# Kernel tuning notes

Measured on AMD Instinct MI355X. Metric: run time of the kernel, lower is better.

The kernel has to match this reference:

```python
import jax, jax.numpy as jnp
import numpy as np

N = 50000
E = 800000
IN_DIM = 256
OUT_DIM = 32
HEADS = 4
HC = OUT_DIM * HEADS  # 128
NEG_SLOPE = 0.2


def _gat_conv(x, src, dst, edge_attr, W, att_src, att_dst, W_e, att_e, b):
    """PyG GATConv (concat=True, edge_dim given, eval mode). src/dst already
    include self loops; edge_attr is [E', 1] with mean-filled self-loop attrs."""
    n = x.shape[0]
    h = (x @ W).reshape(n, HEADS, OUT_DIM)                 # [N,H,C]
    a_s = (h * att_src).sum(-1)                             # [N,H]
    a_d = (h * att_dst).sum(-1)                             # [N,H]
    e = (edge_attr @ W_e).reshape(-1, HEADS, OUT_DIM)       # [E',H,C]
    a_e = (e * att_e).sum(-1)                               # [E',H]
    alpha = jax.nn.leaky_relu(a_s[src] + a_d[dst] + a_e, NEG_SLOPE)
    # softmax over incoming edges per destination node
    m = jax.ops.segment_max(alpha, dst, num_segments=n)
    ex = jnp.exp(alpha - m[dst])
    denom = jax.ops.segment_sum(ex, dst, num_segments=n)
    w = ex / denom[dst]                                     # [E',H]
    out = jax.ops.segment_sum(w[:, :, None] * h[src], dst, num_segments=n)
    return out.reshape(n, HC) + b


def setup_inputs() -> dict:
    key = jax.random.key(0)
    ks = jax.random.split(key, 16)
    x = jax.random.normal(ks[0], (N, IN_DIM), dtype=jnp.float32)
    src = jax.random.randint(ks[1], (E,), 0, N)
    # guarantee no self loops (PyG removes then re-adds them)
    off = jax.random.randint(ks[2], (E,), 1, N)
    dst = (src + off) % N
    edge_index = jnp.stack([src, dst]).astype(jnp.int64)
    edge_weight = jax.random.uniform(ks[3], (E,), dtype=jnp.float32)
    s = 0.1
    params = {
        "W1": jax.random.normal(ks[4], (IN_DIM, HC), jnp.float32) * s,
        "att_src1": jax.random.normal(ks[5], (HEADS, OUT_DIM), jnp.float32) * s,
        "att_dst1": jax.random.normal(ks[6], (HEADS, OUT_DIM), jnp.float32) * s,
        "W_e1": jax.random.normal(ks[7], (1, HC), jnp.float32) * s,
        "att_e1": jax.random.normal(ks[8], (HEADS, OUT_DIM), jnp.float32) * s,
        "b1": jnp.zeros((HC,), jnp.float32),
        "W2": jax.random.normal(ks[9], (HC, HC), jnp.float32) * s,
        "att_src2": jax.random.normal(ks[10], (HEADS, OUT_DIM), jnp.float32) * s,
        "att_dst2": jax.random.normal(ks[11], (HEADS, OUT_DIM), jnp.float32) * s,
        "W_e2": jax.random.normal(ks[12], (1, HC), jnp.float32) * s,
        "att_e2": jax.random.normal(ks[13], (HEADS, OUT_DIM), jnp.float32) * s,
        "b2": jnp.zeros((HC,), jnp.float32),
    }
    return {"x": x, "edge_index": edge_index, "edge_weight": edge_weight, **params}


def reference(x, edge_index, edge_weight,
              W1, att_src1, att_dst1, W_e1, att_e1, b1,
              W2, att_src2, att_dst2, W_e2, att_e2, b2):
    ew = edge_weight[:, None]                               # [E,1]
    # add self loops; self-loop edge_attr = mean of edge_attr (fill_value='mean')
    loop = jnp.arange(N, dtype=edge_index.dtype)
    src = jnp.concatenate([edge_index[0], loop])
    dst = jnp.concatenate([edge_index[1], loop])
    ea = jnp.concatenate([ew, jnp.broadcast_to(ew.mean(0, keepdims=True), (N, 1))])
    h1 = _gat_conv(x, src, dst, ea, W1, att_src1, att_dst1, W_e1, att_e1, b1)
    h2 = _gat_conv(h1, src, dst, ea, W2, att_src2, att_dst2, W_e2, att_e2, b2)
    return h2
```

## Files before the change

### kernel.cpp

```cpp
#include <hip/hip_runtime.h>
#include <hip/hip_fp16.h>

#define N_NODES 50000
#define N_EDGES 800000
#define E_TOT   850000
#define HC 128
#define NEG_SLOPE 0.2f
#define TILE 128
#define KP 40
#define CH 4096
#define NCH ((E_TOT + CH - 1) / CH)
#define NP  ((N_NODES + 255) >> 8)

typedef unsigned short u16;
typedef __attribute__((ext_vector_type(8))) short short8;
typedef __attribute__((ext_vector_type(4))) float f32x4;

__device__ __forceinline__ int edge_get(const void* eidx, int f64, long long i) {
  return f64 ? (int)((const long long*)eidx)[i] : ((const int*)eidx)[i];
}
__device__ __forceinline__ float selh(float4 q, int head) {
  float a = (head & 1) ? q.y : q.x;
  float b = (head & 1) ? q.w : q.z;
  return (head & 2) ? b : a;
}
__device__ __forceinline__ float4 alpha4(float4 as, float4 ad, float w, float4 c) {
  float4 r;
  r.x = as.x + ad.x + w * c.x; r.x = r.x > 0.f ? r.x : NEG_SLOPE * r.x;
  r.y = as.y + ad.y + w * c.y; r.y = r.y > 0.f ? r.y : NEG_SLOPE * r.y;
  r.z = as.z + ad.z + w * c.z; r.z = r.z > 0.f ? r.z : NEG_SLOPE * r.z;
  r.w = as.w + ad.w + w * c.w; r.w = r.w > 0.f ? r.w : NEG_SLOPE * r.w;
  return r;
}
__device__ __forceinline__ void wave_max4(float4& m) {
  #pragma unroll
  for (int o = 1; o < 64; o <<= 1) {
    m.x = fmaxf(m.x, __shfl_xor(m.x, o, 64));
    m.y = fmaxf(m.y, __shfl_xor(m.y, o, 64));
    m.z = fmaxf(m.z, __shfl_xor(m.z, o, 64));
    m.w = fmaxf(m.w, __shfl_xor(m.w, o, 64));
  }
}
__device__ __forceinline__ void wave_sum4(float4& s) {
  #pragma unroll
  for (int o = 1; o < 64; o <<= 1) {
    s.x += __shfl_xor(s.x, o, 64);
    s.y += __shfl_xor(s.y, o, 64);
    s.z += __shfl_xor(s.z, o, 64);
    s.w += __shfl_xor(s.w, o, 64);
  }
}
__device__ __forceinline__ void splitbf(float v, u16& h, u16& l) {
  unsigned b = __float_as_uint(v);
  h = (u16)(b >> 16);
  float lo = v - __uint_as_float(b & 0xFFFF0000u);
  l = (u16)(__float_as_uint(lo) >> 16);
}
__device__ __forceinline__ int block_scan_excl(int val, int* lds) {
  int lane = threadIdx.x & 63, wv = threadIdx.x >> 6;
  int inc = val;
  #pragma unroll
  for (int off = 1; off < 64; off <<= 1) {
    int t = __shfl_up(inc, off, 64);
    if (lane >= off) inc += t;
  }
  if (lane == 63) lds[wv] = inc;
  __syncthreads();
  if (threadIdx.x == 0) {
    int s = 0;
    #pragma unroll
    for (int i = 0; i < 4; ++i) { int t = lds[i]; lds[i] = s; s += t; }
  }
  __syncthreads();
  return lds[wv] + inc - val;
}

__global__ void detect_kernel(const void* eidx, int* flag) {
  const long long* p = (const long long*)eidx;
  long long v = p[threadIdx.x];
  int bad = (v < 0 || v >= N_NODES);
  unsigned long long anybad = __ballot(bad);
  if (threadIdx.x == 0) *flag = (anybad == 0ull);
}

__global__ __launch_bounds__(256) void chunkhist_kernel(const void* eidx,
    const int* __restrict__ flag, const float* __restrict__ ew,
    int* __restrict__ cnt, float* __restrict__ scal) {
  __shared__ int hist[NP];
  __shared__ float sh[4];
  int c = blockIdx.x, tid = threadIdx.x;
  for (int i = tid; i < NP; i += 256) hist[i] = 0;
  __syncthreads();
  int f = *flag;
  int i0 = c * CH, i1 = min(i0 + CH, E_TOT);
  float s = 0.f;
  for (int i = i0 + tid; i < i1; i += 256) {
    int d = (i < N_EDGES) ? edge_get(eidx, f, (long long)N_EDGES + i) : (i - N_EDGES);
    atomicAdd(&hist[d >> 8], 1);
    if (i < N_EDGES) s += ew[i];
  }
  #pragma unroll
  for (int m = 32; m >= 1; m >>= 1) s += __shfl_xor(s, m, 64);
  int lane = tid & 63, wv = tid >> 6;
  if (lane == 0) sh[wv] = s;
  __syncthreads();
  for (int i = tid; i < NP; i += 256) cnt[c * NP + i] = hist[i];
  if (tid == 0) atomicAdd(&scal[0], sh[0] + sh[1] + sh[2] + sh[3]);
}

__global__ __launch_bounds__(256) void colscan_kernel(const int* __restrict__ cnt,
    int* __restrict__ base_rel, int* __restrict__ ptot) {
  __shared__ int lds[4];
  int p = blockIdx.x, c = threadIdx.x;
  int v = (c < NCH) ? cnt[c * NP + p] : 0;
  int e = block_scan_excl(v, lds);
  if (c < NCH) base_rel[c * NP + p] = e;
  if (c == 255) ptot[p] = e;
}

__global__ __launch_bounds__(256) void pscan_prep_kernel(const int* __restrict__ ptot,
    int* __restrict__ pofs, const float* __restrict__ We1, const float* __restrict__ ae1,
    const float* __restrict__ We2, const float* __restrict__ ae2,
    float* __restrict__ scal, float inv_e) {
  __shared__ int lds[4];
  int t = threadIdx.x;
  int v = (t < NP) ? ptot[t] : 0;
  int e = block_scan_excl(v, lds);
  if (t <= NP) pofs[t] = e;
  float p = (t < 128) ? We1[t] * ae1[t] : We2[t - 128] * ae2[t - 128];
  #pragma unroll
  for (int m = 16; m >= 1; m >>= 1) p += __shfl_xor(p, m, 32);
  if ((t & 31) == 0) {
    int hd = (t & 127) >> 5;
    if (t < 128) scal[4 + hd] = p; else scal[8 + hd] = p;
  }
  if (t == 0) scal[1] = scal[0] * inv_e;
}

__global__ __launch_bounds__(256) void partition_kernel(const void* eidx,
    const int* __restrict__ flag, const float* __restrict__ ew,
    const float* __restrict__ scal, const int* __restrict__ base_rel,
    const int* __restrict__ pofs, int2* __restrict__ swp1) {
  __shared__ int cur[NP];
  int c = blockIdx.x, tid = threadIdx.x;
  for (int i = tid; i < NP; i += 256) cur[i] = base_rel[c * NP + i] + pofs[i];
  __syncthreads();
  int f = *flag;
  float wmean = scal[1];
  int i0 = c * CH, i1 = min(i0 + CH, E_TOT);
  for (int i = i0 + tid; i < i1; i += 256) {
    int s, d; float w;
    if (i < N_EDGES) {
      s = edge_get(eidx, f, i);
      d = edge_get(eidx, f, (long long)N_EDGES + i);
      w = ew[i];
    } else {
      s = d = i - N_EDGES;
      w = wmean;
    }
    int pos = atomicAdd(&cur[d >> 8], 1);
    swp1[pos] = make_int2((int)(((unsigned)d << 16) | (unsigned)s), __float_as_int(w));
  }
}

__global__ __launch_bounds__(256) void localsort_kernel(const int2* __restrict__ swp1,
    const int* __restrict__ pofs, int* __restrict__ offs, int2* __restrict__ swp2) {
  __shared__ int lhist[256];
  __shared__ int lds[4];
  int p = blockIdx.x, tid = threadIdx.x;
  int r0 = pofs[p], r1 = pofs[p + 1];
  lhist[tid] = 0;
  __syncthreads();
  for (int i = r0 + tid; i < r1; i += 256) {
    unsigned key = (unsigned)swp1[i].x;
    atomicAdd(&lhist[(key >> 16) & 255u], 1);
  }
  __syncthreads();
  int v = lhist[tid];
  int e = block_scan_excl(v, lds);
  int node = (p << 8) + tid;
  if (node < N_NODES) offs[node] = r0 + e;
  if (p == 0 && tid == 0) offs[N_NODES] = E_TOT;
  lhist[tid] = e;
  __syncthreads();
  for (int i = r0 + tid; i < r1; i += 256) {
    int2 rec = swp1[i];
    unsigned key = (unsigned)rec.x;
    int pos = r0 + atomicAdd(&lhist[(key >> 16) & 255u], 1);
    swp2[pos] = make_int2((int)(key & 0xFFFFu), rec.y);
  }
}

__global__ __launch_bounds__(256) void wprep_kernel(const float* __restrict__ W1,
    const float* __restrict__ W2, u16* __restrict__ w1h, u16* __restrict__ w1l,
    u16* __restrict__ w2h, u16* __restrict__ w2l) {
  int i = blockIdx.x * 256 + threadIdx.x;
  if (i < 128 * 256) {
    int ch = i >> 8, k = i & 255;
    u16 h, l; splitbf(W1[k * 128 + ch], h, l);
    w1h[i] = h; w1l[i] = l;
  } else if (i < 128 * 256 + 128 * 128) {
    int j = i - 128 * 256;
    int ch = j >> 7, k = j & 127;
    u16 h, l; splitbf(W2[k * 128 + ch], h, l);
    w2h[j] = h; w2l[j] = l;
  }
}

__global__ __launch_bounds__(256) void mfma_gemm_kernel(const float* __restrict__ A,
    const u16* __restrict__ wth, const u16* __restrict__ wtl,
    __half* __restrict__ h16, int M, int K) {
  __shared__ u16 Xh[128][KP], Xl[128][KP];
  __shared__ u16 Gh[128][KP], Gl[128][KP];
  int tid  = threadIdx.x;
  int lane = tid & 63, wid = tid >> 6;
  int q = lane >> 4, r = lane & 15;
  int wm = wid >> 1, wn = wid & 1;
  int node0 = blockIdx.x * 128;
  int srow  = tid >> 1;
  int skoff = (tid & 1) << 4;

  f32x4 acc[4][4];
  #pragma unroll
  for (int i = 0; i < 4; ++i)
    #pragma unroll
    for (int j = 0; j < 4; ++j) acc[i][j] = (f32x4)0.f;

  for (int k0 = 0; k0 < K; k0 += 32) {
    int gn = node0 + srow;
    float xv[16];
    if (gn < M) {
      const float* src = A + (size_t)gn * K + k0 + skoff;
      #pragma unroll
      for (int j = 0; j < 4; ++j) {
        float4 t = *(const float4*)(src + j * 4);
        xv[j * 4 + 0] = t.x; xv[j * 4 + 1] = t.y;
        xv[j * 4 + 2] = t.z; xv[j * 4 + 3] = t.w;
      }
    } else {
      #pragma unroll
      for (int j = 0; j < 16; ++j) xv[j] = 0.f;
    }
    const u16* wsrc = wth + (size_t)srow * K + k0 + skoff;
    const u16* lsrc = wtl + (size_t)srow * K + k0 + skoff;
    short8 wh0 = *(const short8*)wsrc;
    short8 wh1 = *(const short8*)(wsrc + 8);
    short8 wl0 = *(const short8*)lsrc;
    short8 wl1 = *(const short8*)(lsrc + 8);
    __syncthreads();
    short8 xh0, xh1, xl0, xl1;
    #pragma unroll
    for (int j = 0; j < 8; ++j) {
      u16 h, l;
      splitbf(xv[j], h, l);     xh0[j] = (short)h; xl0[j] = (short)l;
      splitbf(xv[j + 8], h, l); xh1[j] = (short)h; xl1[j] = (short)l;
    }
    *(short8*)&Xh[srow][skoff]     = xh0;
    *(short8*)&Xh[srow][skoff + 8] = xh1;
    *(short8*)&Xl[srow][skoff]     = xl0;
    *(short8*)&Xl[srow][skoff + 8] = xl1;
    *(short8*)&Gh[srow][skoff]     = wh0;
    *(short8*)&Gh[srow][skoff + 8] = wh1;
    *(short8*)&Gl[srow][skoff]     = wl0;
    *(short8*)&Gl[srow][skoff + 8] = wl1;
    __syncthreads();
    short8 ah[4], al[4], bh[4], bl[4];
    #pragma unroll
    for (int mi = 0; mi < 4; ++mi) {
      int row = wm * 64 + mi * 16 + r;
      ah[mi] = *(const short8*)&Gh[row][q * 8];
      al[mi] = *(const short8*)&Gl[row][q * 8];
    }
    #pragma unroll
    for (int ni = 0; ni < 4; ++ni) {
      int row = wn * 64 + ni * 16 + r;
      bh[ni] = *(const short8*)&Xh[row][q * 8];
      bl[ni] = *(const short8*)&Xl[row][q * 8];
    }
    #pragma unroll
    for (int mi = 0; mi < 4; ++mi)
      #pragma unroll
      for (int ni = 0; ni < 4; ++ni) {
        acc[mi][ni] = __builtin_amdgcn_mfma_f32_16x16x32_bf16(ah[mi], bh[ni], acc[mi][ni], 0, 0, 0);
        acc[mi][ni] = __builtin_amdgcn_mfma_f32_16x16x32_bf16(ah[mi], bl[ni], acc[mi][ni], 0, 0, 0);
        acc[mi][ni] = __builtin_amdgcn_mfma_f32_16x16x32_bf16(al[mi], bh[ni], acc[mi][ni], 0, 0, 0);
      }
  }
  #pragma unroll
  for (int ni = 0; ni < 4; ++ni) {
    int node = node0 + wn * 64 + ni * 16 + r;
    if (node < M) {
      #pragma unroll
      for (int mi = 0; mi < 4; ++mi) {
        int chb = wm * 64 + mi * 16 + q * 4;
        __half hh[4];
        hh[0] = __float2half(acc[mi][ni][0]);
        hh[1] = __float2half(acc[mi][ni][1]);
        hh[2] = __float2half(acc[mi][ni][2]);
        hh[3] = __float2half(acc[mi][ni][3]);
        *(float2*)(h16 + (size_t)node * HC + chb) = *(float2*)hh;
      }
    }
  }
}

__global__ __launch_bounds__(256) void attn_coef16_kernel(const __half* __restrict__ h,
    const float* __restrict__ att_s, const float* __restrict__ att_d,
    float* __restrict__ a_s, float* __restrict__ a_d, int n) {
  int lane = threadIdx.x & 63, wid = threadIdx.x >> 6;
  int node = blockIdx.x * 4 + wid;
  if (node >= n) return;
  __half2 hv = *(const __half2*)(h + (size_t)node * HC + 2 * lane);
  float v0 = __low2float(hv), v1 = __high2float(hv);
  float2 as2 = *(const float2*)(att_s + 2 * lane);
  float2 ad2 = *(const float2*)(att_d + 2 * lane);
  float ps = v0 * as2.x + v1 * as2.y;
  float pd = v0 * ad2.x + v1 * ad2.y;
  #pragma unroll
  for (int o = 1; o < 16; o <<= 1) {
    ps += __shfl_xor(ps, o, 64);
    pd += __shfl_xor(pd, o, 64);
  }
  if ((lane & 15) == 0) {
    a_s[(size_t)node * 4 + (lane >> 4)] = ps;
    a_d[(size_t)node * 4 + (lane >> 4)] = pd;
  }
}

__global__ __launch_bounds__(256) void aggregate_kernel(const __half* __restrict__ h,
    const int2* __restrict__ swp, const int* __restrict__ offs,
    const float* __restrict__ a_s, const float* __restrict__ a_d,
    const float* __restrict__ cptr, const float* __restrict__ bias,
    float* __restrict__ out, int n) {
  __shared__ float4 wals[4][TILE];
  __shared__ int    ssh[4][TILE];
  int lane = threadIdx.x & 63;
  int wv   = threadIdx.x >> 6;
  int v    = blockIdx.x * 4 + wv;
  if (v >= n) return;
  int r0  = offs[v];
  int deg = offs[v + 1] - r0;
  float4 c  = *(const float4*)cptr;
  float4 ad = *(const float4*)(a_d + (size_t)v * 4);
  int head  = lane >> 4;
  float2 acc = make_float2(0.f, 0.f);
  const __half* hb = h + 2 * lane;
  float4 mx = make_float4(-INFINITY, -INFINITY, -INFINITY, -INFINITY);
  float4 sm = make_float4(0.f, 0.f, 0.f, 0.f);

  if (deg <= TILE) {
    for (int i = lane; i < deg; i += 64) {
      int2 sw = swp[r0 + i];
      float w = __int_as_float(sw.y);
      float4 as = *(const float4*)(a_s + (size_t)sw.x * 4);
      float4 al = alpha4(as, ad, w, c);
      wals[wv][i] = al; ssh[wv][i] = sw.x;
      mx.x = fmaxf(mx.x, al.x); mx.y = fmaxf(mx.y, al.y);
      mx.z = fmaxf(mx.z, al.z); mx.w = fmaxf(mx.w, al.w);
    }
    wave_max4(mx);
    for (int i = lane; i < deg; i += 64) {
      float4 al = wals[wv][i];
      float4 e;
      e.x = expf(al.x - mx.x); e.y = expf(al.y - mx.y);
      e.z = expf(al.z - mx.z); e.w = expf(al.w - mx.w);
      wals[wv][i] = e;
      sm.x += e.x; sm.y += e.y; sm.z += e.z; sm.w += e.w;
    }
    wave_sum4(sm);
    int i = 0;
    for (; i + 8 <= deg; i += 8) {
      float wr[8]; int sr[8];
      #pragma unroll
      for (int j = 0; j < 8; ++j) {
        sr[j] = ssh[wv][i + j];
        wr[j] = ((const float*)&wals[wv][i + j])[head];
      }
      __half2 hv[8];
      #pragma unroll
      for (int j = 0; j < 8; ++j)
        hv[j] = *(const __half2*)(hb + (size_t)sr[j] * HC);
      #pragma unroll
      for (int j = 0; j < 8; ++j) {
        acc.x += wr[j] * __low2float(hv[j]);
        acc.y += wr[j] * __high2float(hv[j]);
      }
    }
    for (; i < deg; ++i) {
      int s0 = ssh[wv][i];
      float w0 = ((const float*)&wals[wv][i])[head];
      __half2 hvv = *(const __half2*)(hb + (size_t)s0 * HC);
      acc.x += w0 * __low2float(hvv);
      acc.y += w0 * __high2float(hvv);
    }
  } else {
    for (int i = lane; i < deg; i += 64) {
      int2 sw = swp[r0 + i];
      float4 as = *(const float4*)(a_s + (size_t)sw.x * 4);
      float4 al = alpha4(as, ad, __int_as_float(sw.y), c);
      mx.x = fmaxf(mx.x, al.x); mx.y = fmaxf(mx.y, al.y);
      mx.z = fmaxf(mx.z, al.z); mx.w = fmaxf(mx.w, al.w);
    }
    wave_max4(mx);
    for (int i = lane; i < deg; i += 64) {
      int2 sw = swp[r0 + i];
      float4 as = *(const float4*)(a_s + (size_t)sw.x * 4);
      float4 al = alpha4(as, ad, __int_as_float(sw.y), c);
      sm.x += expf(al.x - mx.x); sm.y += expf(al.y - mx.y);
      sm.z += expf(al.z - mx.z); sm.w += expf(al.w - mx.w);
    }
    wave_sum4(sm);
    float mxh = selh(mx, head);
    for (int i = 0; i < deg; ++i) {
      int2 sw = swp[r0 + i];
      float4 as = *(const float4*)(a_s + (size_t)sw.x * 4);
      float4 al = alpha4(as, ad, __int_as_float(sw.y), c);
      float e = expf(selh(al, head) - mxh);
      __half2 hvv = *(const __half2*)(hb + (size_t)sw.x * HC);
      acc.x += e * __low2float(hvv);
      acc.y += e * __high2float(hvv);
    }
  }
  float inv = 1.0f / selh(sm, head);
  float2 bb = *(const float2*)(bias + 2 * lane);
  float2 r;
  r.x = acc.x * inv + bb.x;
  r.y = acc.y * inv + bb.y;
  *(float2*)(out + (size_t)v * HC + 2 * lane) = r;
}

extern "C" void kernel_launch(void* const* d_in, const int* in_sizes, int n_in,
                              void* d_out, int out_size, void* d_ws, size_t ws_size,
                              hipStream_t stream) {
  const float* x   = (const float*)d_in[0];
  const void*  ei  = d_in[1];
  const float* ew  = (const float*)d_in[2];
  const float* W1  = (const float*)d_in[3];
  const float* as1 = (const float*)d_in[4];
  const float* ad1 = (const float*)d_in[5];
  const float* We1 = (const float*)d_in[6];
  const float* ae1 = (const float*)d_in[7];
  const float* b1  = (const float*)d_in[8];
  const float* W2  = (const float*)d_in[9];
  const float* as2 = (const float*)d_in[10];
  const float* ad2 = (const float*)d_in[11];
  const float* We2 = (const float*)d_in[12];
  const float* ae2 = (const float*)d_in[13];
  const float* b2  = (const float*)d_in[14];
  float* out = (float*)d_out;

  char* p = (char*)d_ws;
  auto alloc = [&](size_t b) { char* r = p; p += (b + 255) & ~(size_t)255; return r; };
  float*  scal     = (float*)alloc(256);
  __half* h16      = (__half*)alloc((size_t)N_NODES * HC * 2);
  float*  out1     = (float*)alloc((size_t)N_NODES * HC * 4);
  float*  a_s      = (float*)alloc((size_t)N_NODES * 4 * 4);
  float*  a_d      = (float*)alloc((size_t)N_NODES * 4 * 4);
  int*    offs     = (int*)alloc((size_t)(N_NODES + 1) * 4);
  int*    cnt      = (int*)alloc((size_t)NCH * NP * 4);
  int*    base_rel = (int*)alloc((size_t)NCH * NP * 4);
  int*    ptot     = (int*)alloc((size_t)NP * 4);
  int*    pofs     = (int*)alloc((size_t)(NP + 1) * 4);
  int2*   swp1     = (int2*)alloc((size_t)E_TOT * 8);
  int2*   swp2     = (int2*)alloc((size_t)E_TOT * 8);
  u16*    w1h      = (u16*)alloc((size_t)128 * 256 * 2);
  u16*    w1l      = (u16*)alloc((size_t)128 * 256 * 2);
  u16*    w2h      = (u16*)alloc((size_t)128 * 128 * 2);
  u16*    w2l      = (u16*)alloc((size_t)128 * 128 * 2);

  hipMemsetAsync(scal, 0, 256, stream);

  int* flag = (int*)scal + 16;

  detect_kernel<<<1, 64, 0, stream>>>(ei, flag);
  chunkhist_kernel<<<NCH, 256, 0, stream>>>(ei, flag, ew, cnt, scal);
  colscan_kernel<<<NP, 256, 0, stream>>>(cnt, base_rel, ptot);
  pscan_prep_kernel<<<1, 256, 0, stream>>>(ptot, pofs, We1, ae1, We2, ae2, scal,
                                           1.0f / N_EDGES);
  partition_kernel<<<NCH, 256, 0, stream>>>(ei, flag, ew, scal, base_rel, pofs, swp1);
  localsort_kernel<<<NP, 256, 0, stream>>>(swp1, pofs, offs, swp2);
  wprep_kernel<<<192, 256, 0, stream>>>(W1, W2, w1h, w1l, w2h, w2l);

  const int ggrid = (N_NODES + 127) / 128;
  const int agrid = (N_NODES + 3) / 4;
  mfma_gemm_kernel<<<ggrid, 256, 0, stream>>>(x, w1h, w1l, h16, N_NODES, 256);
  attn_coef16_kernel<<<agrid, 256, 0, stream>>>(h16, as1, ad1, a_s, a_d, N_NODES);
  aggregate_kernel<<<agrid, 256, 0, stream>>>(h16, swp2, offs, a_s, a_d, scal + 4, b1,
                                              out1, N_NODES);
  mfma_gemm_kernel<<<ggrid, 256, 0, stream>>>(out1, w2h, w2l, h16, N_NODES, 128);
  attn_coef16_kernel<<<agrid, 256, 0, stream>>>(h16, as2, ad2, a_s, a_d, N_NODES);
  aggregate_kernel<<<agrid, 256, 0, stream>>>(h16, swp2, offs, a_s, a_d, scal + 8, b2,
                                              out, N_NODES);
}
```

Before: 298.7 us.

## Fuse attention coefficients into GEMM epilogue, inline index detection, widen gather unroll

Computes the per-node a_s/a_d attention dot products directly from the MFMA accumulators in the GEMM epilogue, which removes the separate attn_coef kernel and its reread of h16. The index-dtype detection kernel is folded into chunkhist and partition, so each block redoes a 64-element check instead of paying for an extra launch. The aggregate gather loop now unrolls 16 loads per step with masked tails instead of 8 plus a scalar remainder, aiming for more memory parallelism. The trade-offs are a heavier GEMM epilogue with extra registers and shuffles, and some wasted loads on the padded tail of short neighbour lists.

```diff
diff --git a/kernel.cpp b/kernel.cpp
--- a/kernel.cpp
+++ b/kernel.cpp
@@ -74,24 +74,26 @@
   __syncthreads();
   return lds[wv] + inc - val;
 }
-
-__global__ void detect_kernel(const void* eidx, int* flag) {
-  const long long* p = (const long long*)eidx;
-  long long v = p[threadIdx.x];
-  int bad = (v < 0 || v >= N_NODES);
-  unsigned long long anybad = __ballot(bad);
-  if (threadIdx.x == 0) *flag = (anybad == 0ull);
+__device__ __forceinline__ int local_detect(const void* eidx, int* f_sh) {
+  int tid = threadIdx.x;
+  if (tid < 64) {
+    long long v = ((const long long*)eidx)[tid];
+    int bad = (v < 0 || v >= N_NODES);
+    unsigned long long anybad = __ballot(bad);
+    if (tid == 0) *f_sh = (anybad == 0ull);
+  }
+  __syncthreads();
+  return *f_sh;
 }
 
 __global__ __launch_bounds__(256) void chunkhist_kernel(const void* eidx,
-    const int* __restrict__ flag, const float* __restrict__ ew,
-    int* __restrict__ cnt, float* __restrict__ scal) {
+    const float* __restrict__ ew, int* __restrict__ cnt, float* __restrict__ scal) {
   __shared__ int hist[NP];
   __shared__ float sh[4];
+  __shared__ int f_sh;
   int c = blockIdx.x, tid = threadIdx.x;
   for (int i = tid; i < NP; i += 256) hist[i] = 0;
-  __syncthreads();
-  int f = *flag;
+  int f = local_detect(eidx, &f_sh);
   int i0 = c * CH, i1 = min(i0 + CH, E_TOT);
   float s = 0.f;
   for (int i = i0 + tid; i < i1; i += 256) {
@@ -138,14 +140,14 @@
 }
 
 __global__ __launch_bounds__(256) void partition_kernel(const void* eidx,
-    const int* __restrict__ flag, const float* __restrict__ ew,
-    const float* __restrict__ scal, const int* __restrict__ base_rel,
-    const int* __restrict__ pofs, int2* __restrict__ swp1) {
+    const float* __restrict__ ew, const float* __restrict__ scal,
+    const int* __restrict__ base_rel, const int* __restrict__ pofs,
+    int2* __restrict__ swp1) {
   __shared__ int cur[NP];
+  __shared__ int f_sh;
   int c = blockIdx.x, tid = threadIdx.x;
   for (int i = tid; i < NP; i += 256) cur[i] = base_rel[c * NP + i] + pofs[i];
-  __syncthreads();
-  int f = *flag;
+  int f = local_detect(eidx, &f_sh);
   float wmean = scal[1];
   int i0 = c * CH, i1 = min(i0 + CH, E_TOT);
   for (int i = i0 + tid; i < i1; i += 256) {
@@ -209,7 +211,9 @@
 
 __global__ __launch_bounds__(256) void mfma_gemm_kernel(const float* __restrict__ A,
     const u16* __restrict__ wth, const u16* __restrict__ wtl,
-    __half* __restrict__ h16, int M, int K) {
+    const float* __restrict__ att_s, const float* __restrict__ att_d,
+    __half* __restrict__ h16, float* __restrict__ a_s, float* __restrict__ a_d,
+    int M, int K) {
   __shared__ u16 Xh[128][KP], Xl[128][KP];
   __shared__ u16 Gh[128][KP], Gl[128][KP];
   int tid  = threadIdx.x;
@@ -286,6 +290,12 @@
         acc[mi][ni] = __builtin_amdgcn_mfma_f32_16x16x32_bf16(al[mi], bh[ni], acc[mi][ni], 0, 0, 0);
       }
   }
+  float4 sv[4], dv[4];
+  #pragma unroll
+  for (int mi = 0; mi < 4; ++mi) {
+    sv[mi] = *(const float4*)(att_s + wm * 64 + mi * 16 + q * 4);
+    dv[mi] = *(const float4*)(att_d + wm * 64 + mi * 16 + q * 4);
+  }
   #pragma unroll
   for (int ni = 0; ni < 4; ++ni) {
     int node = node0 + wn * 64 + ni * 16 + r;
@@ -301,29 +311,31 @@
         *(float2*)(h16 + (size_t)node * HC + chb) = *(float2*)hh;
       }
     }
-  }
-}
-
-__global__ __launch_bounds__(256) void attn_coef16_kernel(const __half* __restrict__ h,
-    const float* __restrict__ att_s, const float* __restrict__ att_d,
-    float* __restrict__ a_s, float* __restrict__ a_d, int n) {
-  int lane = threadIdx.x & 63, wid = threadIdx.x >> 6;
-  int node = blockIdx.x * 4 + wid;
-  if (node >= n) return;
-  __half2 hv = *(const __half2*)(h + (size_t)node * HC + 2 * lane);
-  float v0 = __low2float(hv), v1 = __high2float(hv);
-  float2 as2 = *(const float2*)(att_s + 2 * lane);
-  float2 ad2 = *(const float2*)(att_d + 2 * lane);
-  float ps = v0 * as2.x + v1 * as2.y;
-  float pd = v0 * ad2.x + v1 * ad2.y;
-  #pragma unroll
-  for (int o = 1; o < 16; o <<= 1) {
-    ps += __shfl_xor(ps, o, 64);
-    pd += __shfl_xor(pd, o, 64);
-  }
-  if ((lane & 15) == 0) {
-    a_s[(size_t)node * 4 + (lane >> 4)] = ps;
-    a_d[(size_t)node * 4 + (lane >> 4)] = pd;
+    float ps0 = 0.f, pd0 = 0.f, ps1 = 0.f, pd1 = 0.f;
+    #pragma unroll
+    for (int mi = 0; mi < 2; ++mi)
+      #pragma unroll
+      for (int t = 0; t < 4; ++t) {
+        float av = acc[mi][ni][t];
+        ps0 += av * ((const float*)&sv[mi])[t];
+        pd0 += av * ((const float*)&dv[mi])[t];
+      }
+    #pragma unroll
+    for (int mi = 2; mi < 4; ++mi)
+      #pragma unroll
+      for (int t = 0; t < 4; ++t) {
+        float av = acc[mi][ni][t];
+        ps1 += av * ((const float*)&sv[mi])[t];
+        pd1 += av * ((const float*)&dv[mi])[t];
+      }
+    ps0 += __shfl_xor(ps0, 16, 64); ps0 += __shfl_xor(ps0, 32, 64);
+    pd0 += __shfl_xor(pd0, 16, 64); pd0 += __shfl_xor(pd0, 32, 64);
+    ps1 += __shfl_xor(ps1, 16, 64); ps1 += __shfl_xor(ps1, 32, 64);
+    pd1 += __shfl_xor(pd1, 16, 64); pd1 += __shfl_xor(pd1, 32, 64);
+    if (q == 0 && node < M) {
+      *(float2*)(a_s + (size_t)node * 4 + wm * 2) = make_float2(ps0, ps1);
+      *(float2*)(a_d + (size_t)node * 4 + wm * 2) = make_float2(pd0, pd1);
+    }
   }
 }
 
@@ -368,30 +380,25 @@
       sm.x += e.x; sm.y += e.y; sm.z += e.z; sm.w += e.w;
     }
     wave_sum4(sm);
-    int i = 0;
-    for (; i + 8 <= deg; i += 8) {
-      float wr[8]; int sr[8];
-      #pragma unroll
-      for (int j = 0; j < 8; ++j) {
-        sr[j] = ssh[wv][i + j];
-        wr[j] = ((const float*)&wals[wv][i + j])[head];
-      }
-      __half2 hv[8];
-      #pragma unroll
-      for (int j = 0; j < 8; ++j)
+    for (int i = 0; i < deg; i += 16) {
+      float wr[16]; int sr[16];
+      #pragma unroll
+      for (int j = 0; j < 16; ++j) {
+        int idx = i + j;
+        bool ok = idx < deg;
+        int ii = ok ? idx : i;
+        sr[j] = ssh[wv][ii];
+        wr[j] = ok ? ((const float*)&wals[wv][ii])[head] : 0.f;
+      }
+      __half2 hv[16];
+      #pragma unroll
+      for (int j = 0; j < 16; ++j)
         hv[j] = *(const __half2*)(hb + (size_t)sr[j] * HC);
       #pragma unroll
-      for (int j = 0; j < 8; ++j) {
+      for (int j = 0; j < 16; ++j) {
         acc.x += wr[j] * __low2float(hv[j]);
         acc.y += wr[j] * __high2float(hv[j]);
       }
-    }
-    for (; i < deg; ++i) {
-      int s0 = ssh[wv][i];
-      float w0 = ((const float*)&wals[wv][i])[head];
-      __half2 hvv = *(const __half2*)(hb + (size_t)s0 * HC);
-      acc.x += w0 * __low2float(hvv);
-      acc.y += w0 * __high2float(hvv);
     }
   } else {
     for (int i = lane; i < deg; i += 64) {
@@ -470,25 +477,22 @@
 
   hipMemsetAsync(scal, 0, 256, stream);
 
-  int* flag = (int*)scal + 16;
-
-  detect_kernel<<<1, 64, 0, stream>>>(ei, flag);
-  chunkhist_kernel<<<NCH, 256, 0, stream>>>(ei, flag, ew, cnt, scal);
+  chunkhist_kernel<<<NCH, 256, 0, stream>>>(ei, ew, cnt, scal);
   colscan_kernel<<<NP, 256, 0, stream>>>(cnt, base_rel, ptot);
   pscan_prep_kernel<<<1, 256, 0, stream>>>(ptot, pofs, We1, ae1, We2, ae2, scal,
                                            1.0f / N_EDGES);
-  partition_kernel<<<NCH, 256, 0, stream>>>(ei, flag, ew, scal, base_rel, pofs, swp1);
+  partition_kernel<<<NCH, 256, 0, stream>>>(ei, ew, scal, base_rel, pofs, swp1);
   localsort_kernel<<<NP, 256, 0, stream>>>(swp1, pofs, offs, swp2);
   wprep_kernel<<<192, 256, 0, stream>>>(W1, W2, w1h, w1l, w2h, w2l);
 
   const int ggrid = (N_NODES + 127) / 128;
   const int agrid = (N_NODES + 3) / 4;
-  mfma_gemm_kernel<<<ggrid, 256, 0, stream>>>(x, w1h, w1l, h16, N_NODES, 256);
-  attn_coef16_kernel<<<agrid, 256, 0, stream>>>(h16, as1, ad1, a_s, a_d, N_NODES);
+  mfma_gemm_kernel<<<ggrid, 256, 0, stream>>>(x, w1h, w1l, as1, ad1, h16, a_s, a_d,
+                                              N_NODES, 256);
   aggregate_kernel<<<agrid, 256, 0, stream>>>(h16, swp2, offs, a_s, a_d, scal + 4, b1,
                                               out1, N_NODES);
-  mfma_gemm_kernel<<<ggrid, 256, 0, stream>>>(out1, w2h, w2l, h16, N_NODES, 128);
-  attn_coef16_kernel<<<agrid, 256, 0, stream>>>(h16, as2, ad2, a_s, a_d, N_NODES);
+  mfma_gemm_kernel<<<ggrid, 256, 0, stream>>>(out1, w2h, w2l, as2, ad2, h16, a_s, a_d,
+                                              N_NODES, 128);
   aggregate_kernel<<<agrid, 256, 0, stream>>>(h16, swp2, offs, a_s, a_d, scal + 8, b2,
                                               out, N_NODES);
 }
```

Measured after the change: 293.9 us. Within noise of the previous version (-1.6%).
